# Optimization experiments

Measured on AMD Instinct MI355X. Metric: run time of the kernel, lower is better.

## Reference

```python
import jax, jax.numpy as jnp
import numpy as np
import itertools

N_OBJECTS = 6  # subsets of range(6), sizes 1..6 -> 63 subsets

def _subset_groups():
    # group subsets by length so each group runs as one batched LSTM
    groups = {}
    for m in range(1, N_OBJECTS + 1):
        for s in itertools.combinations(range(6), m):
            groups.setdefault(m, []).append(list(s))
    return [(m, np.asarray(v, dtype=np.int32)) for m, v in groups.items()]

SUBSET_GROUPS = _subset_groups()


def _lstm_final_h(x, W_ih, W_hh, b_ih, b_hh):
    """x: [B,T,D] -> final hidden state [B,H]. PyTorch gate order i,f,g,o."""
    H = W_hh.shape[1]
    B = x.shape[0]
    # precompute input projections for all timesteps: [B,T,4H]
    xz = jnp.einsum('btd,gd->btg', x, W_ih) + b_ih + b_hh

    def step(carry, xt):
        h, c = carry
        z = xt + h @ W_hh.T
        i, f, g, o = jnp.split(z, 4, axis=-1)
        c = jax.nn.sigmoid(f) * c + jax.nn.sigmoid(i) * jnp.tanh(g)
        h = jax.nn.sigmoid(o) * jnp.tanh(c)
        return (h, c), None

    h0 = jnp.zeros((B, H), x.dtype)
    (h, _), _ = jax.lax.scan(step, (h0, h0), jnp.swapaxes(xz, 0, 1))
    return h


def setup_inputs() -> dict:
    key = jax.random.key(0)
    ks = jax.random.split(key, 10)
    D, H, FC, A = 16, 128, 256, 10
    mb = 8192
    s = lambda k, shape, fan: jax.random.normal(k, shape, jnp.float32) * (1.0 / np.sqrt(fan))
    return {
        'x_input': jax.random.normal(ks[0], (mb, 6, D), jnp.float32),
        'W_ih': s(ks[1], (4 * H, D), D),
        'W_hh': s(ks[2], (4 * H, H), H),
        'b_ih': jnp.zeros((4 * H,), jnp.float32),
        'b_hh': jnp.zeros((4 * H,), jnp.float32),
        'fc1_W': s(ks[3], (FC, H), H),
        'fc1_b': jnp.zeros((FC,), jnp.float32),
        'fc2_W': s(ks[4], (A, FC), FC),
        'fc2_b': jnp.zeros((A,), jnp.float32),
    }


def reference(x_input, W_ih, W_hh, b_ih, b_hh, fc1_W, fc1_b, fc2_W, fc2_b):
    mb = x_input.shape[0]
    H = W_hh.shape[1]
    hs = []
    # subsets of the same length are batched into one LSTM pass (fused form of
    # the original 63-iteration python loop); aggregation is permutation-invariant
    for m, idx in SUBSET_GROUPS:
        nL = idx.shape[0]
        xg = x_input[:, idx, :]                       # [mb, nL, m, D] gather
        xg = xg.reshape(mb * nL, m, x_input.shape[-1])
        h = _lstm_final_h(xg, W_ih, W_hh, b_ih, b_hh)  # [mb*nL, H]
        hs.append(h.reshape(mb, nL, H))
    holder = jnp.concatenate(hs, axis=1)              # [mb, 63, H]
    x = jnp.max(holder, axis=1)                       # aggregate == 'max'
    x = jax.nn.relu(x @ fc1_W.T + fc1_b)
    x = x @ fc2_W.T + fc2_b
    return jax.nn.log_softmax(x, axis=-1)
```

## Files before the change

kernel.cpp:

```cpp
#include <hip/hip_runtime.h>
#include <hip/hip_bf16.h>

#define BLOCK   512
#define NSAMP   16
#define HDIM    128
#define DDIM    16
#define NOBJ    6
#define NSLOT   14

typedef __attribute__((ext_vector_type(8))) short bf16x8;
typedef __attribute__((ext_vector_type(4))) float f32x4;

constexpr int pc6(int m)  { int c = 0; for (int i = 0; i < 6; ++i) c += (m >> i) & 1; return c; }
constexpr int msb6(int m) { int b = -1; for (int i = 0; i < 6; ++i) if (m & (1 << i)) b = i; return b; }

struct PNode { int jo, ps, sl; bool bar; };
struct Plan2 { PNode nd[63]; int lvlStart[8]; };
constexpr Plan2 make_plan2() {
    Plan2 P{};
    int slotOf[64] = {};
    bool busy[NSLOT] = {};
    int k = 0;
    for (int d = 1; d <= 6; ++d) {
        P.lvlStart[d] = k;
        for (int M = 1; M < 64; ++M) {
            if (pc6(M) != d || msb6(M) != 5) continue;
            P.nd[k].jo = 5;
            P.nd[k].ps = (d == 1) ? -1 : slotOf[M & ~(1 << 5)];
            P.nd[k].sl = -1;
            P.nd[k].bar = false;
            ++k;
        }
        int pend[20] = {}; int np = 0;
        for (int M = 1; M < 64; ++M)
            if (pc6(M) == d && msb6(M) < 5) pend[np++] = M;
        int key[20] = {};
        for (int i = 0; i < np; ++i) {
            if (d == 1) { key[i] = 0; continue; }
            const int par = pend[i] & ~(1 << msb6(pend[i]));
            int c2 = 0;
            for (int j2 = 0; j2 < np; ++j2)
                if ((pend[j2] & ~(1 << msb6(pend[j2]))) == par) ++c2;
            key[i] = c2;
        }
        for (int a = 0; a < np; ++a)
            for (int b2 = a + 1; b2 < np; ++b2)
                if (key[b2] < key[a]) {
                    int tm = key[a]; key[a] = key[b2]; key[b2] = tm;
                    tm = pend[a]; pend[a] = pend[b2]; pend[b2] = tm;
                }
        bool placed[20] = {};
        int nplaced = 0;
        bool firstPhase = true;
        while (nplaced < np) {
            bool needBar = !firstPhase;
            bool any = false;
            for (int i = 0; i < np; ++i) {
                if (placed[i]) continue;
                int fs = -1;
                for (int s = 0; s < NSLOT; ++s) if (!busy[s]) { fs = s; break; }
                if (fs < 0) break;
                const int M = pend[i]; const int hi = msb6(M);
                busy[fs] = true; slotOf[M] = fs;
                P.nd[k].jo = hi;
                P.nd[k].ps = (d == 1) ? -1 : slotOf[M & ~(1 << hi)];
                P.nd[k].sl = fs;
                P.nd[k].bar = needBar; needBar = false;
                ++k; placed[i] = true; ++nplaced; any = true;
            }
            firstPhase = false;
            if (nplaced < np) {
                if (!any) break;
                for (int M = 1; M < 64; ++M) {
                    if (pc6(M) != d - 1 || msb6(M) >= 5) continue;
                    bool allp = true;
                    for (int i = 0; i < np; ++i)
                        if (!placed[i] &&
                            ((pend[i] & ~(1 << msb6(pend[i]))) == M)) allp = false;
                    if (allp) busy[slotOf[M]] = false;
                }
            }
        }
        for (int s = 0; s < NSLOT; ++s) busy[s] = false;
        for (int M = 1; M < 64; ++M)
            if (pc6(M) == d && msb6(M) < 5) busy[slotOf[M]] = true;
    }
    P.lvlStart[7] = k;
    return P;
}
constexpr Plan2 PL2 = make_plan2();
static_assert(PL2.lvlStart[7] == 63, "plan must cover all 63 nodes");

#define LOG2E   1.44269504f
#define TWOL2E  2.88539008f
#define SLOT_SH 2048

__device__ __forceinline__ unsigned short f2bf(float x) {
    union { float f; unsigned int u; } a; a.f = x;
    unsigned int r = (a.u + 0x7FFFu + ((a.u >> 16) & 1u)) >> 16;
    return (unsigned short)r;
}
__device__ __forceinline__ unsigned pk2(float a, float b) {
    union { __hip_bfloat162 h; unsigned u; } z;
    z.h = __float22bfloat162_rn(float2{a, b});
    return z.u;
}
__device__ __forceinline__ float bflo(unsigned p) {
    union { unsigned u; float f; } a; a.u = p << 16; return a.f;
}
__device__ __forceinline__ float bfhi(unsigned p) {
    union { unsigned u; float f; } a; a.u = p & 0xFFFF0000u; return a.f;
}


__global__ __launch_bounds__(BLOCK)
__attribute__((amdgpu_waves_per_eu(2, 4)))
void subset_lstm_l14_kernel(
    const float* __restrict__ x_input,
    const float* __restrict__ W_ih,
    const float* __restrict__ W_hh,
    const float* __restrict__ b_ih,
    const float* __restrict__ b_hh,
    const float* __restrict__ fc1_W,
    const float* __restrict__ fc1_b,
    const float* __restrict__ fc2_W,
    const float* __restrict__ fc2_b,
    float* __restrict__ out)
{
    __shared__ __align__(16) unsigned short hs[NSLOT * SLOT_SH];
    __shared__ __align__(16) unsigned short xb[NOBJ * 2 * NSAMP * 8];
    __shared__ __align__(16) unsigned short xpad[16];
    float* s_maxh  = (float*)hs;
    float* s_fc1   = (float*)(hs + 4096);
    float* s_logit = (float*)xb;

    const int t      = threadIdx.x;
    const int w      = t >> 6;
    const int lane   = t & 63;
    const int quad   = lane >> 4;
    const int m16    = lane & 15;
    const int s_base = blockIdx.x * NSAMP;

    if (t < 16) xpad[t] = (t == 0) ? f2bf(1.0f) : (unsigned short)0;

    for (int idx = t; idx < NOBJ * 2 * NSAMP * 8; idx += BLOCK) {
        const int j = idx & 7, n = (idx >> 3) & 15, q = (idx >> 7) & 1, obj = idx >> 8;
        xb[idx] = f2bf(x_input[(s_base + n) * (NOBJ * DDIM) + obj * DDIM + q * 8 + j]);
    }

    bf16x8 wf[4][5];
    #pragma unroll
    for (int g = 0; g < 4; ++g) {
        const float sc = (g == 2) ? TWOL2E : -LOG2E;
        const int grow = g * HDIM + w * 16 + m16;
        const float* whr = W_hh + grow * HDIM;
        const float* wir = W_ih + grow * DDIM;
        #pragma unroll
        for (int q = 0; q < 4; ++q) {
            union { unsigned short u[8]; bf16x8 v; } pk;
            #pragma unroll
            for (int j = 0; j < 8; ++j)
                pk.u[j] = f2bf(sc * whr[q * 32 + quad * 8 + j]);
            wf[g][q] = pk.v;
        }
        {
            union { unsigned short u[8]; bf16x8 v; } pk;
            #pragma unroll
            for (int j = 0; j < 8; ++j) {
                float v = 0.0f;
                if (quad < 2) v = sc * wir[quad * 8 + j];
                else if (quad == 2 && j == 0) v = sc * (b_ih[grow] + b_hh[grow]);
                pk.u[j] = f2bf(v);
            }
            wf[g][4] = pk.v;
        }
    }

    uint2 cs[NSLOT];
    float mh[4] = {-1e30f, -1e30f, -1e30f, -1e30f};
    const int kslot = w * 2 + (quad >> 1);

    #pragma unroll
    for (int d = 1; d <= 6; ++d) {
        __syncthreads();
        #pragma unroll
        for (int k = PL2.lvlStart[d]; k < PL2.lvlStart[d + 1]; ++k) {
            if (PL2.nd[k].bar) __syncthreads();
            const int jo = PL2.nd[k].jo;
            const int ps = PL2.nd[k].ps;
            const int sl = PL2.nd[k].sl;

            f32x4 acc[4];
            #pragma unroll
            for (int g = 0; g < 4; ++g)
                acc[g] = f32x4{0.f, 0.f, 0.f, 0.f};

            {
                const unsigned short* bp = (quad < 2)
                    ? &xb[((jo * 2 + quad) * NSAMP + m16) * 8]
                    : &xpad[(quad - 2) * 8];
                const bf16x8 bfx = *(const bf16x8*)bp;
                #pragma unroll
                for (int g = 0; g < 4; ++g)
                    acc[g] = __builtin_amdgcn_mfma_f32_16x16x32_bf16(
                        wf[g][4], bfx, acc[g], 0, 0, 0);
            }
            if (ps >= 0) {
                #pragma unroll
                for (int q = 0; q < 4; ++q) {
                    const bf16x8 bh = *(const bf16x8*)
                        &hs[((ps * 16 + q * 4 + quad) * NSAMP + m16) * 8];
                    #pragma unroll
                    for (int g = 0; g < 4; ++g)
                        acc[g] = __builtin_amdgcn_mfma_f32_16x16x32_bf16(
                            wf[g][q], bh, acc[g], 0, 0, 0);
                }
            }

            float cn4[4], hn4[4];
            #pragma unroll
            for (int r = 0; r < 4; ++r) {
                float cprev = 0.0f;
                if (ps >= 0) {
                    const unsigned p = (r < 2) ? cs[ps].x : cs[ps].y;
                    cprev = (r & 1) ? bfhi(p) : bflo(p);
                }
                const float u  = 1.0f + __builtin_amdgcn_exp2f(acc[0][r]);
                const float q  = 1.0f + __builtin_amdgcn_exp2f(acc[1][r]);
                const float v  = 1.0f + __builtin_amdgcn_exp2f(acc[2][r]);
                const float qo = 1.0f + __builtin_amdgcn_exp2f(acc[3][r]);
                const float uv  = u * v;
                const float num = fmaf(q, v - 2.0f, cprev * uv);
                const float cn  = num * __builtin_amdgcn_rcpf(q * uv);
                const float wt  = 1.0f + __builtin_amdgcn_exp2f(TWOL2E * cn);
                const float h   = (wt - 2.0f) * __builtin_amdgcn_rcpf(qo * wt);
                cn4[r] = cn; hn4[r] = h;
                mh[r] = fmaxf(mh[r], h);
            }

            if (sl >= 0) {
                cs[sl].x = pk2(cn4[0], cn4[1]);
                cs[sl].y = pk2(cn4[2], cn4[3]);
                union { __hip_bfloat162 h2[2]; uint2 v; } hp;
                hp.h2[0] = __float22bfloat162_rn(float2{hn4[0], hn4[1]});
                hp.h2[1] = __float22bfloat162_rn(float2{hn4[2], hn4[3]});
                *(uint2*)&hs[((sl * 16 + kslot) * NSAMP + m16) * 8
                             + (quad & 1) * 4] = hp.v;
            }
        }
    }

    __syncthreads();
    {
        float4 v; v.x = mh[0]; v.y = mh[1]; v.z = mh[2]; v.w = mh[3];
        *(float4*)&s_maxh[m16 * HDIM + w * 16 + quad * 4] = v;
    }
    __syncthreads();

    {
        const int f  = t & 255;
        const int sh = t >> 8;
        float a1[8];
        #pragma unroll
        for (int s = 0; s < 8; ++s) a1[s] = fc1_b[f];
        for (int k4 = 0; k4 < HDIM / 4; ++k4) {
            const float4 wv = *(const float4*)&fc1_W[f * HDIM + k4 * 4];
            #pragma unroll
            for (int s = 0; s < 8; ++s) {
                const float4 h4 = *(const float4*)&s_maxh[(sh * 8 + s) * HDIM + k4 * 4];
                a1[s] += wv.x * h4.x + wv.y * h4.y + wv.z * h4.z + wv.w * h4.w;
            }
        }
        #pragma unroll
        for (int s = 0; s < 8; ++s)
            s_fc1[(sh * 8 + s) * 256 + f] = fmaxf(a1[s], 0.0f);
    }
    __syncthreads();

    if (t < NSAMP * 10) {
        const int s = t / 10, a = t % 10;
        float acc2 = fc2_b[a];
        for (int f4 = 0; f4 < 256 / 4; ++f4) {
            const float4 wv = *(const float4*)&fc2_W[a * 256 + f4 * 4];
            const float4 v  = *(const float4*)&s_fc1[s * 256 + f4 * 4];
            acc2 += wv.x * v.x + wv.y * v.y + wv.z * v.z + wv.w * v.w;
        }
        s_logit[s * 10 + a] = acc2;
    }
    __syncthreads();

    if (t < NSAMP) {
        float m = -1e30f;
        #pragma unroll
        for (int a = 0; a < 10; ++a) m = fmaxf(m, s_logit[t * 10 + a]);
        float sum = 0.0f;
        #pragma unroll
        for (int a = 0; a < 10; ++a) sum += __expf(s_logit[t * 10 + a] - m);
        const float lse = m + __logf(sum);
        #pragma unroll
        for (int a = 0; a < 10; ++a)
            out[(s_base + t) * 10 + a] = s_logit[t * 10 + a] - lse;
    }
}

extern "C" void kernel_launch(void* const* d_in, const int* in_sizes, int n_in,
                              void* d_out, int out_size, void* d_ws, size_t ws_size,
                              hipStream_t stream)
{
    (void)d_ws; (void)ws_size; (void)n_in; (void)out_size;

    const float* x   = (const float*)d_in[0];
    const float* Wih = (const float*)d_in[1];
    const float* Whh = (const float*)d_in[2];
    const float* bih = (const float*)d_in[3];
    const float* bhh = (const float*)d_in[4];
    const float* f1w = (const float*)d_in[5];
    const float* f1b = (const float*)d_in[6];
    const float* f2w = (const float*)d_in[7];
    const float* f2b = (const float*)d_in[8];

    const int mb = in_sizes[0] / (NOBJ * DDIM);
    dim3 grid(mb / NSAMP), block(BLOCK);
    subset_lstm_l14_kernel<<<grid, block, 0, stream>>>(
        x, Wih, Whh, bih, bhh, f1w, f1b, f2w, f2b, (float*)d_out);
}
```

Baseline: 196.9 us.

## Precompute per-object input projections once and keep cell state in LDS

The input-projection MFMA (W_ih·x plus bias) is computed once per object before the subset tree walk and held in registers as xz[6][4]. Each node then seeds its accumulators from xz instead of redoing that MFMA, which removes one MFMA per gate per node. The per-slot cell state moves from a 14-entry register array to a shared-memory buffer, which frees registers for the xz array but adds LDS reads and writes. The waves-per-EU hint is pinned to 2 and the xb layout is widened to hold the bias-padding lanes.

```diff
diff --git a/kernel.cpp b/kernel.cpp
--- a/kernel.cpp
+++ b/kernel.cpp
@@ -114,8 +114,8 @@
 
 
 __global__ __launch_bounds__(BLOCK)
-__attribute__((amdgpu_waves_per_eu(2, 4)))
-void subset_lstm_l14_kernel(
+__attribute__((amdgpu_waves_per_eu(2, 2)))
+void subset_lstm_xz_kernel(
     const float* __restrict__ x_input,
     const float* __restrict__ W_ih,
     const float* __restrict__ W_hh,
@@ -127,9 +127,9 @@
     const float* __restrict__ fc2_b,
     float* __restrict__ out)
 {
-    __shared__ __align__(16) unsigned short hs[NSLOT * SLOT_SH];
-    __shared__ __align__(16) unsigned short xb[NOBJ * 2 * NSAMP * 8];
-    __shared__ __align__(16) unsigned short xpad[16];
+    __shared__ __align__(16) unsigned short hs [NSLOT * SLOT_SH];
+    __shared__ __align__(16) unsigned short csb[NSLOT * SLOT_SH];
+    __shared__ __align__(16) unsigned short xb[NOBJ * 4 * NSAMP * 8];
     float* s_maxh  = (float*)hs;
     float* s_fc1   = (float*)(hs + 4096);
     float* s_logit = (float*)xb;
@@ -141,20 +141,20 @@
     const int m16    = lane & 15;
     const int s_base = blockIdx.x * NSAMP;
 
-    if (t < 16) xpad[t] = (t == 0) ? f2bf(1.0f) : (unsigned short)0;
-
-    for (int idx = t; idx < NOBJ * 2 * NSAMP * 8; idx += BLOCK) {
-        const int j = idx & 7, n = (idx >> 3) & 15, q = (idx >> 7) & 1, obj = idx >> 8;
-        xb[idx] = f2bf(x_input[(s_base + n) * (NOBJ * DDIM) + obj * DDIM + q * 8 + j]);
-    }
-
-    bf16x8 wf[4][5];
+    for (int idx = t; idx < NOBJ * 4 * NSAMP * 8; idx += BLOCK) {
+        const int j = idx & 7, n = (idx >> 3) & 15, q = (idx >> 7) & 3, obj = idx >> 9;
+        float v;
+        if (q < 2) v = x_input[(s_base + n) * (NOBJ * DDIM) + obj * DDIM + q * 8 + j];
+        else       v = (q == 2 && j == 0) ? 1.0f : 0.0f;
+        xb[idx] = f2bf(v);
+    }
+
+    bf16x8 wf[4][4];
     #pragma unroll
     for (int g = 0; g < 4; ++g) {
         const float sc = (g == 2) ? TWOL2E : -LOG2E;
         const int grow = g * HDIM + w * 16 + m16;
         const float* whr = W_hh + grow * HDIM;
-        const float* wir = W_ih + grow * DDIM;
         #pragma unroll
         for (int q = 0; q < 4; ++q) {
             union { unsigned short u[8]; bf16x8 v; } pk;
@@ -163,7 +163,22 @@
                 pk.u[j] = f2bf(sc * whr[q * 32 + quad * 8 + j]);
             wf[g][q] = pk.v;
         }
-        {
+    }
+
+    __syncthreads();
+
+    f32x4 xz[NOBJ][4];
+    {
+        bf16x8 bfx[NOBJ];
+        #pragma unroll
+        for (int o = 0; o < NOBJ; ++o)
+            bfx[o] = *(const bf16x8*)&xb[((o * 4 + quad) * NSAMP + m16) * 8];
+        const f32x4 fz = {0.f, 0.f, 0.f, 0.f};
+        #pragma unroll
+        for (int g = 0; g < 4; ++g) {
+            const float sc = (g == 2) ? TWOL2E : -LOG2E;
+            const int grow = g * HDIM + w * 16 + m16;
+            const float* wir = W_ih + grow * DDIM;
             union { unsigned short u[8]; bf16x8 v; } pk;
             #pragma unroll
             for (int j = 0; j < 8; ++j) {
@@ -172,13 +187,16 @@
                 else if (quad == 2 && j == 0) v = sc * (b_ih[grow] + b_hh[grow]);
                 pk.u[j] = f2bf(v);
             }
-            wf[g][4] = pk.v;
-        }
-    }
-
-    uint2 cs[NSLOT];
+            #pragma unroll
+            for (int o = 0; o < NOBJ; ++o)
+                xz[o][g] = __builtin_amdgcn_mfma_f32_16x16x32_bf16(
+                    pk.v, bfx[o], fz, 0, 0, 0);
+        }
+    }
+
     float mh[4] = {-1e30f, -1e30f, -1e30f, -1e30f};
     const int kslot = w * 2 + (quad >> 1);
+    unsigned short* const c_lane = &csb[(((w * 4 + quad) * NSAMP) + m16) * 4];
 
     #pragma unroll
     for (int d = 1; d <= 6; ++d) {
@@ -190,24 +208,22 @@
             const int ps = PL2.nd[k].ps;
             const int sl = PL2.nd[k].sl;
 
+            float cp[4] = {0.f, 0.f, 0.f, 0.f};
             f32x4 acc[4];
-            #pragma unroll
-            for (int g = 0; g < 4; ++g)
-                acc[g] = f32x4{0.f, 0.f, 0.f, 0.f};
-
-            {
-                const unsigned short* bp = (quad < 2)
-                    ? &xb[((jo * 2 + quad) * NSAMP + m16) * 8]
-                    : &xpad[(quad - 2) * 8];
-                const bf16x8 bfx = *(const bf16x8*)bp;
+            if (ps >= 0) {
+                const uint2 cpk = *(const uint2*)(c_lane + ps * SLOT_SH);
+                cp[0] = bflo(cpk.x); cp[1] = bfhi(cpk.x);
+                cp[2] = bflo(cpk.y); cp[3] = bfhi(cpk.y);
+                {
+                    const bf16x8 bh = *(const bf16x8*)
+                        &hs[((ps * 16 + 0 * 4 + quad) * NSAMP + m16) * 8];
+                    #pragma unroll
+                    for (int g = 0; g < 4; ++g)
+                        acc[g] = __builtin_amdgcn_mfma_f32_16x16x32_bf16(
+                            wf[g][0], bh, xz[jo][g], 0, 0, 0);
+                }
                 #pragma unroll
-                for (int g = 0; g < 4; ++g)
-                    acc[g] = __builtin_amdgcn_mfma_f32_16x16x32_bf16(
-                        wf[g][4], bfx, acc[g], 0, 0, 0);
-            }
-            if (ps >= 0) {
-                #pragma unroll
-                for (int q = 0; q < 4; ++q) {
+                for (int q = 1; q < 4; ++q) {
                     const bf16x8 bh = *(const bf16x8*)
                         &hs[((ps * 16 + q * 4 + quad) * NSAMP + m16) * 8];
                     #pragma unroll
@@ -215,22 +231,20 @@
                         acc[g] = __builtin_amdgcn_mfma_f32_16x16x32_bf16(
                             wf[g][q], bh, acc[g], 0, 0, 0);
                 }
+            } else {
+                #pragma unroll
+                for (int g = 0; g < 4; ++g) acc[g] = xz[jo][g];
             }
 
             float cn4[4], hn4[4];
             #pragma unroll
             for (int r = 0; r < 4; ++r) {
-                float cprev = 0.0f;
-                if (ps >= 0) {
-                    const unsigned p = (r < 2) ? cs[ps].x : cs[ps].y;
-                    cprev = (r & 1) ? bfhi(p) : bflo(p);
-                }
                 const float u  = 1.0f + __builtin_amdgcn_exp2f(acc[0][r]);
                 const float q  = 1.0f + __builtin_amdgcn_exp2f(acc[1][r]);
                 const float v  = 1.0f + __builtin_amdgcn_exp2f(acc[2][r]);
                 const float qo = 1.0f + __builtin_amdgcn_exp2f(acc[3][r]);
                 const float uv  = u * v;
-                const float num = fmaf(q, v - 2.0f, cprev * uv);
+                const float num = fmaf(q, v - 2.0f, cp[r] * uv);
                 const float cn  = num * __builtin_amdgcn_rcpf(q * uv);
                 const float wt  = 1.0f + __builtin_amdgcn_exp2f(TWOL2E * cn);
                 const float h   = (wt - 2.0f) * __builtin_amdgcn_rcpf(qo * wt);
@@ -239,13 +253,11 @@
             }
 
             if (sl >= 0) {
-                cs[sl].x = pk2(cn4[0], cn4[1]);
-                cs[sl].y = pk2(cn4[2], cn4[3]);
-                union { __hip_bfloat162 h2[2]; uint2 v; } hp;
-                hp.h2[0] = __float22bfloat162_rn(float2{hn4[0], hn4[1]});
-                hp.h2[1] = __float22bfloat162_rn(float2{hn4[2], hn4[3]});
+                uint2 cw; cw.x = pk2(cn4[0], cn4[1]); cw.y = pk2(cn4[2], cn4[3]);
+                *(uint2*)(c_lane + sl * SLOT_SH) = cw;
+                uint2 hw; hw.x = pk2(hn4[0], hn4[1]); hw.y = pk2(hn4[2], hn4[3]);
                 *(uint2*)&hs[((sl * 16 + kslot) * NSAMP + m16) * 8
-                             + (quad & 1) * 4] = hp.v;
+                             + (quad & 1) * 4] = hw;
             }
         }
     }
@@ -321,6 +333,6 @@
 
     const int mb = in_sizes[0] / (NOBJ * DDIM);
     dim3 grid(mb / NSAMP), block(BLOCK);
-    subset_lstm_l14_kernel<<<grid, block, 0, stream>>>(
+    subset_lstm_xz_kernel<<<grid, block, 0, stream>>>(
         x, Wih, Whh, bih, bhh, f1w, f1b, f2w, f2b, (float*)d_out);
 }
```

New measurement: 205.6 us. +4.4%, slower.
